# Performance work log

Measured on AMD Instinct MI355X. Metric: run time of the kernel, lower is better.

The kernel has to match this reference:

```python
import jax, jax.numpy as jnp
import numpy as np
import itertools

B, T, C, H = 2, 2048, 1024, 8
HD = C // H  # head_dim = 128


def _head_dirs():
    # 8 trigrams = vertices of cube {-1,+1}^3, L2-normalized (norm sqrt(3))
    signs = [-1.0, 1.0]
    tri = np.array(list(itertools.product(signs, repeat=3)), dtype=np.float32)
    tri = tri / np.linalg.norm(tri, axis=1, keepdims=True)
    return jnp.asarray(tri[:H])  # [H, 3]


def setup_inputs() -> dict:
    key = jax.random.key(0)
    ks = jax.random.split(key, 5)
    w = lambda k, sh: jax.random.normal(k, sh, dtype=jnp.float32) * 0.02
    return {
        "x": jax.random.normal(ks[0], (B, T, C), dtype=jnp.float32),
        "Wq": w(ks[1], (H * 3, C)),
        "Wk": w(ks[2], (H * 3, C)),
        "Wv": w(ks[3], (C, C)),
        "Wo": w(ks[4], (C, C)),
        "scale": jnp.asarray(1.0 / np.sqrt(3.0), dtype=jnp.float32),
    }


def reference(x, Wq, Wk, Wv, Wo, scale):
    Bb, Tt, Cc = x.shape
    dirs = _head_dirs()  # [H, 3] constant buffer
    # tiny 3-dim per-head Q/K projections
    q3 = (x @ Wq.T).reshape(Bb, Tt, H, 3).transpose(0, 2, 1, 3)  # [B,H,T,3]
    k3 = (x @ Wk.T).reshape(Bb, Tt, H, 3).transpose(0, 2, 1, 3)  # [B,H,T,3]
    v = (x @ Wv.T).reshape(Bb, Tt, H, HD).transpose(0, 2, 1, 3)  # [B,H,T,HD]
    # projections of q/k onto each head's trigram direction
    q_on_dir = jnp.einsum('bhtd,hd->bht', q3, dirs)  # [B,H,T]
    k_on_dir = jnp.einsum('bhtd,hd->bht', k3, dirs)  # [B,H,T]
    # scores = scaled 3-dim dot product + geometric outer-product bias
    scores = jnp.einsum('bhtd,bhsd->bhts', q3, k3) * scale \
        + q_on_dir[..., :, None] * k_on_dir[..., None, :]  # [B,H,T,T]
    causal = jnp.tril(jnp.ones((Tt, Tt), dtype=bool))
    scores = jnp.where(causal, scores, -jnp.inf)
    attn = jax.nn.softmax(scores, axis=-1)
    out = jnp.einsum('bhts,bhsd->bhtd', attn, v)  # [B,H,T,HD]
    out = out.transpose(0, 2, 1, 3).reshape(Bb, Tt, Cc)
    return out @ Wo.T
```

## Files before the change

kernel.cpp:

```cpp
#include <hip/hip_runtime.h>
#include <hip/hip_bf16.h>

#define B_  2
#define T_  2048
#define C_  1024
#define H_  8
#define HD_ 128
#define M_  (B_*T_)

typedef short  bf16x8 __attribute__((ext_vector_type(8)));
typedef float  f32x4  __attribute__((ext_vector_type(4)));
typedef unsigned short u16x8 __attribute__((ext_vector_type(8)));
typedef unsigned int   u32x4 __attribute__((ext_vector_type(4)));

typedef const __attribute__((address_space(1))) void* gas_ptr;
typedef __attribute__((address_space(3))) void*       las_ptr;

#define L2E_ 1.4426950408889634f

static __device__ __forceinline__ unsigned short f2bf(float f) {
    unsigned int u = __float_as_uint(f);
    u += 0x7fffu + ((u >> 16) & 1u);
    return (unsigned short)(u >> 16);
}
static __device__ __forceinline__ unsigned int rne_u32(float f) {
    unsigned int u = __float_as_uint(f);
    return u + 0x7fffu + ((u >> 16) & 1u);
}
static __device__ __forceinline__ float bf2f(unsigned short u) {
    return __uint_as_float(((unsigned int)u) << 16);
}
static __device__ __forceinline__ float exp2_fast(float x) {
#if __has_builtin(__builtin_amdgcn_exp2f)
    return __builtin_amdgcn_exp2f(x);
#else
    return exp2f(x);
#endif
}

__global__ __launch_bounds__(256) void k_proj_qk(const float* __restrict__ x,
                                                 const float* __restrict__ Wq,
                                                 const float* __restrict__ Wk,
                                                 const float* __restrict__ Wv,
                                                 const float* __restrict__ Wo,
                                                 const float* __restrict__ scale_p,
                                                 float* __restrict__ qt,
                                                 float* __restrict__ kt,
                                                 unsigned short* __restrict__ xbf,
                                                 unsigned short* __restrict__ wvbf,
                                                 unsigned short* __restrict__ wobf) {
    __shared__ __align__(16) float wl[48][260];
    __shared__ __align__(16) float xl[16][260];
    __shared__ float res[16][48];
    const int tid  = threadIdx.x;

    if (blockIdx.x >= (M_ / 16)) {
        int i = (blockIdx.x - M_ / 16) * 256 + tid;
        const float* src; unsigned short* dst; int off;
        if (i < 262144) { src = Wv; dst = wvbf; off = i; }
        else            { src = Wo; dst = wobf; off = i - 262144; }
        float4 v = reinterpret_cast<const float4*>(src)[off];
        ushort4 o;
        o.x = f2bf(v.x); o.y = f2bf(v.y); o.z = f2bf(v.z); o.w = f2bf(v.w);
        reinterpret_cast<ushort4*>(dst)[off] = o;
        return;
    }

    const int row0 = blockIdx.x << 4;
    const int r    = tid >> 4, sub = tid & 15;
    float a0 = 0.f, a1 = 0.f, a2 = 0.f;

    for (int ch = 0; ch < 4; ++ch) {
        const int k0 = ch * 256;
        #pragma unroll
        for (int i = 0; i < 12; ++i) {
            int fi = i * 256 + tid;
            int wr = fi >> 6, wc = (fi & 63) * 4;
            const float* src = (wr < 24) ? (Wq + (size_t)wr * C_) : (Wk + (size_t)(wr - 24) * C_);
            *reinterpret_cast<float4*>(&wl[wr][wc]) = *reinterpret_cast<const float4*>(src + k0 + wc);
        }
        #pragma unroll
        for (int i = 0; i < 4; ++i) {
            int fi = i * 256 + tid;
            int xr = fi >> 6, xc = (fi & 63) * 4;
            size_t goff = (size_t)(row0 + xr) * C_ + k0 + xc;
            float4 xv = *reinterpret_cast<const float4*>(x + goff);
            *reinterpret_cast<float4*>(&xl[xr][xc]) = xv;
            ushort4 o;
            o.x = f2bf(xv.x); o.y = f2bf(xv.y); o.z = f2bf(xv.z); o.w = f2bf(xv.w);
            *reinterpret_cast<ushort4*>(xbf + goff) = o;
        }
        __syncthreads();
        const int oc = sub * 3;
        #pragma unroll 4
        for (int k = 0; k < 256; k += 4) {
            float4 xv = *reinterpret_cast<const float4*>(&xl[r][k]);
            float4 w0 = *reinterpret_cast<const float4*>(&wl[oc + 0][k]);
            float4 w1 = *reinterpret_cast<const float4*>(&wl[oc + 1][k]);
            float4 w2 = *reinterpret_cast<const float4*>(&wl[oc + 2][k]);
            a0 += xv.x * w0.x + xv.y * w0.y + xv.z * w0.z + xv.w * w0.w;
            a1 += xv.x * w1.x + xv.y * w1.y + xv.z * w1.z + xv.w * w1.w;
            a2 += xv.x * w2.x + xv.y * w2.y + xv.z * w2.z + xv.w * w2.w;
        }
        __syncthreads();
    }
    res[r][sub * 3 + 0] = a0;
    res[r][sub * 3 + 1] = a1;
    res[r][sub * 3 + 2] = a2;
    __syncthreads();

    {
        const int rr = tid >> 4, s2 = tid & 15;
        const int isK = s2 >> 3, h = s2 & 7;
        const float r3 = 0.57735026918962576f;
        float d0 = (h & 4) ? r3 : -r3;
        float d1 = (h & 2) ? r3 : -r3;
        float d2 = (h & 1) ? r3 : -r3;
        const float* v3 = &res[rr][isK * 24 + h * 3];
        float a = v3[0], b = v3[1], c = v3[2];
        float ond = a * d0 + b * d1 + c * d2;
        float sc = scale_p[0];
        float4 ov = isK ? make_float4(a, b, c, ond)
                        : make_float4(a * sc * L2E_, b * sc * L2E_, c * sc * L2E_, ond * L2E_);
        float* dst = isK ? kt : qt;
        int grow = row0 + rr;
        int b_ = grow >> 11, t_idx = grow & (T_ - 1);
        reinterpret_cast<float4*>(dst)[(size_t)(b_ * H_ + h) * T_ + t_idx] = ov;
    }
}

template <int MODE>
__global__ __launch_bounds__(256) void k_gemm128x64(const unsigned short* __restrict__ A,
                                                    const unsigned short* __restrict__ Bw,
                                                    void* __restrict__ Cout,
                                                    int Mdim, int Ndim, int Kdim) {
    __shared__ __align__(16) unsigned short lds_a[8][128][8];
    __shared__ __align__(16) unsigned short lds_b[8][64][8];
    const int tid = threadIdx.x;
    const int nbn = Ndim >> 6;
    const int cpx = (int)gridDim.x >> 3;
    const int bidx = (blockIdx.x & 7) * cpx + (blockIdx.x >> 3);
    const int bm = (bidx / nbn) << 7;
    const int bn = (bidx % nbn) << 6;
    const int w = tid >> 6, l = tid & 63;
    const int wm = (w >> 1) << 6, wn = (w & 1) << 5;
    const int lh = l & 15, lq = l >> 4;

    f32x4 acc[4][2];
    #pragma unroll
    for (int i = 0; i < 4; ++i)
        #pragma unroll
        for (int j = 0; j < 2; ++j)
            acc[i][j] = (f32x4){0.f, 0.f, 0.f, 0.f};

    for (int k0 = 0; k0 < Kdim; k0 += 64) {
        #pragma unroll
        for (int p = 0; p < 4; ++p) {
            int flat = p * 256 + tid;
            int kq = flat >> 7, row = flat & 127;
            __builtin_amdgcn_global_load_lds((gas_ptr)(A + (size_t)(bm + row) * Kdim + k0 + kq * 8),
                (las_ptr)(&lds_a[0][0][0] + (size_t)flat * 8), 16, 0, 0);
        }
        #pragma unroll
        for (int p = 0; p < 2; ++p) {
            int flat = p * 256 + tid;
            int kq = flat >> 6, row = flat & 63;
            __builtin_amdgcn_global_load_lds((gas_ptr)(Bw + (size_t)(bn + row) * Kdim + k0 + kq * 8),
                (las_ptr)(&lds_b[0][0][0] + (size_t)flat * 8), 16, 0, 0);
        }
        __syncthreads();

        #pragma unroll
        for (int kk = 0; kk < 2; ++kk) {
            bf16x8 af[4], bfr[2];
            #pragma unroll
            for (int f = 0; f < 4; ++f)
                af[f] = *reinterpret_cast<const bf16x8*>(&lds_a[lq + 4 * kk][wm + f * 16 + lh][0]);
            #pragma unroll
            for (int f = 0; f < 2; ++f)
                bfr[f] = *reinterpret_cast<const bf16x8*>(&lds_b[lq + 4 * kk][wn + f * 16 + lh][0]);
            #pragma unroll
            for (int i = 0; i < 4; ++i)
                #pragma unroll
                for (int j = 0; j < 2; ++j)
                    acc[i][j] = __builtin_amdgcn_mfma_f32_16x16x32_bf16(af[i], bfr[j], acc[i][j], 0, 0, 0);
        }
        __syncthreads();
    }

    if constexpr (MODE == 0) {
        float* Cf = (float*)Cout;
        #pragma unroll
        for (int i = 0; i < 4; ++i) {
            int rbase = bm + wm + i * 16 + lq * 4;
            #pragma unroll
            for (int j = 0; j < 2; ++j) {
                int cidx = bn + wn + j * 16 + lh;
                #pragma unroll
                for (int r = 0; r < 4; ++r)
                    Cf[(size_t)(rbase + r) * Ndim + cidx] = acc[i][j][r];
            }
        }
    } else {
        __shared__ unsigned short ldsT[128][72];
        #pragma unroll
        for (int i = 0; i < 4; ++i)
            #pragma unroll
            for (int j = 0; j < 2; ++j)
                #pragma unroll
                for (int r = 0; r < 4; ++r)
                    ldsT[wm + i * 16 + lq * 4 + r][wn + j * 16 + lh] = f2bf(acc[i][j][r]);
        __syncthreads();
        unsigned short* vt_out = (unsigned short*)Cout;
        int c = tid & 63, part = tid >> 6;
        int b = bm >> 11, t0 = bm & (T_ - 1);
        unsigned short* dst = vt_out + ((size_t)b * C_ + bn + c) * T_ + t0 + part * 32;
        #pragma unroll
        for (int jj = 0; jj < 4; ++jj) {
            u16x8 v;
            #pragma unroll
            for (int k = 0; k < 8; ++k) v[k] = ldsT[part * 32 + jj * 8 + k][c];
            *reinterpret_cast<u16x8*>(dst + jj * 8) = v;
        }
    }
}

__global__ __launch_bounds__(256) void k_attn64(
        const float4* __restrict__ qt, const float4* __restrict__ kt,
        const unsigned short* __restrict__ vt,
        unsigned short* __restrict__ mpart,
        float2* __restrict__ mlbuf,
        int nsp, int lg2nsp) {
    __shared__ __align__(16) unsigned short lv[2][8192];
    __shared__ __align__(16) float4 lk[2][64];
    const int tid = threadIdx.x;
    const int w = tid >> 6, l = tid & 63;
    const int lh = l & 15, lg = l >> 4;
    const int bid = blockIdx.x;
    const int qb = 31 - (bid >> (4 + lg2nsp));
    const int sp = (bid >> 4) & (nsp - 1);
    const int bh = bid & 15;
    const int q0 = qb << 6;
    const int qrow = q0 + 4 * lh + w;
    const int nt = qb + 1;

    const float4* qtb = qt + (size_t)bh * T_;
    const float4* ktb = kt + (size_t)bh * T_;
    const unsigned short* vtb = vt + (size_t)bh * HD_ * T_;

    const unsigned short* vsrc[4];
    #pragma unroll
    for (int i = 0; i < 4; ++i) {
        int f = i * 256 + tid;
        vsrc[i] = vtb + (size_t)((((f >> 6) & 7) * 16) + (f & 15)) * T_
                      + ((f >> 9) << 5) + ((f >> 4) & 3) * 8;
    }

#define STAGE(ST, BUF) do {                                                    \
    int s0_ = (ST) << 6;                                                       \
    __builtin_amdgcn_global_load_lds((gas_ptr)(vsrc[0] + s0_),                 \
        (las_ptr)(&lv[BUF][0] + (size_t)(0 * 256 + tid) * 8), 16, 0, 0);       \
    __builtin_amdgcn_global_load_lds((gas_ptr)(vsrc[1] + s0_),                 \
        (las_ptr)(&lv[BUF][0] + (size_t)(1 * 256 + tid) * 8), 16, 0, 0);       \
    __builtin_amdgcn_global_load_lds((gas_ptr)(vsrc[2] + s0_),                 \
        (las_ptr)(&lv[BUF][0] + (size_t)(2 * 256 + tid) * 8), 16, 0, 0);       \
    __builtin_amdgcn_global_load_lds((gas_ptr)(vsrc[3] + s0_),                 \
        (las_ptr)(&lv[BUF][0] + (size_t)(3 * 256 + tid) * 8), 16, 0, 0);       \
    __builtin_amdgcn_global_load_lds((gas_ptr)(ktb + s0_ + l),                 \
        (las_ptr)(&lk[BUF][0]), 16, 0, 0);                                     \
} while (0)

    const float4 q4 = qtb[qrow];
    f32x4 acc[8];
    #pragma unroll
    for (int n = 0; n < 8; ++n) acc[n] = (f32x4){0.f, 0.f, 0.f, 0.f};
    float m = -1e30f, lsum = 0.f;

    if (sp < nt)       STAGE(sp, 0);
    if (sp + nsp < nt) STAGE(sp + nsp, 1);
    __syncthreads();

    int buf = 0;
    for (int st = sp; st < nt; st += nsp) {
        const int s0 = st << 6;
        const int c0 = s0 + lg * 8;
        const int c1 = s0 + 32 + lg * 8;

        float p[16];
        if (st != qb) {
            #pragma unroll
            for (int jj = 0; jj < 8; ++jj) {
                float4 k4 = lk[buf][lg * 8 + jj];
                p[jj] = fmaf(q4.x, k4.x, fmaf(q4.y, k4.y, fmaf(q4.z, k4.z, q4.w * k4.w)));
            }
            #pragma unroll
            for (int jj = 0; jj < 8; ++jj) {
                float4 k4 = lk[buf][32 + lg * 8 + jj];
                p[8 + jj] = fmaf(q4.x, k4.x, fmaf(q4.y, k4.y, fmaf(q4.z, k4.z, q4.w * k4.w)));
            }
        } else {
            #pragma unroll
            for (int jj = 0; jj < 8; ++jj) {
                float4 k4 = lk[buf][lg * 8 + jj];
                float sc = fmaf(q4.x, k4.x, fmaf(q4.y, k4.y, fmaf(q4.z, k4.z, q4.w * k4.w)));
                p[jj] = (c0 + jj > qrow) ? -1e30f : sc;
            }
            #pragma unroll
            for (int jj = 0; jj < 8; ++jj) {
                float4 k4 = lk[buf][32 + lg * 8 + jj];
                float sc = fmaf(q4.x, k4.x, fmaf(q4.y, k4.y, fmaf(q4.z, k4.z, q4.w * k4.w)));
                p[8 + jj] = (c1 + jj > qrow) ? -1e30f : sc;
            }
        }

        float ma = fmaxf(fmaxf(p[0], p[1]), p[2]);
        float mb = fmaxf(fmaxf(p[3], p[4]), p[5]);
        float mc = fmaxf(fmaxf(p[6], p[7]), p[8]);
        float md = fmaxf(fmaxf(p[9], p[10]), p[11]);
        float me = fmaxf(fmaxf(p[12], p[13]), p[14]);
        float mt = fmaxf(fmaxf(fmaxf(ma, mb), fmaxf(mc, md)), fmaxf(me, p[15]));
        mt = fmaxf(mt, __shfl_xor(mt, 16));
        mt = fmaxf(mt, __shfl_xor(mt, 32));
        if (__any(mt > m + 8.f)) {
            float mnew = fmaxf(m, mt);
            float corr = exp2_fast(m - mnew);
            m = mnew;
            lsum *= corr;
            float cc0 = __shfl(corr, 4 * lg + 0);
            float cc1 = __shfl(corr, 4 * lg + 1);
            float cc2 = __shfl(corr, 4 * lg + 2);
            float cc3 = __shfl(corr, 4 * lg + 3);
            #pragma unroll
            for (int n = 0; n < 8; ++n) {
                acc[n][0] *= cc0; acc[n][1] *= cc1; acc[n][2] *= cc2; acc[n][3] *= cc3;
            }
        }
        #pragma unroll
        for (int jj = 0; jj < 16; ++jj)
            p[jj] = exp2_fast(p[jj] - m);
        float sa = (p[0] + p[1] + p[2]) + (p[3] + p[4] + p[5]);
        float sb = (p[6] + p[7] + p[8]) + (p[9] + p[10] + p[11]);
        float ps = sa + sb + ((p[12] + p[13] + p[14]) + p[15]);
        ps += __shfl_xor(ps, 16);
        ps += __shfl_xor(ps, 32);
        lsum += ps;

        u32x4 w0, w1;
        #pragma unroll
        for (int i = 0; i < 4; ++i) {
            w0[i] = __builtin_amdgcn_perm(rne_u32(p[2 * i + 1]), rne_u32(p[2 * i]), 0x07060302u);
            w1[i] = __builtin_amdgcn_perm(rne_u32(p[8 + 2 * i + 1]), rne_u32(p[8 + 2 * i]), 0x07060302u);
        }
        bf16x8 pa0 = __builtin_bit_cast(bf16x8, w0);
        bf16x8 pa1 = __builtin_bit_cast(bf16x8, w1);

        #pragma unroll
        for (int n = 0; n < 8; ++n) {
            bf16x8 vf = *reinterpret_cast<const bf16x8*>(&lv[buf][(size_t)(n * 64 + lg * 16 + lh) * 8]);
            acc[n] = __builtin_amdgcn_mfma_f32_16x16x32_bf16(pa0, vf, acc[n], 0, 0, 0);
        }
        #pragma unroll
        for (int n = 0; n < 8; ++n) {
            bf16x8 vf = *reinterpret_cast<const bf16x8*>(&lv[buf][(size_t)(512 + n * 64 + lg * 16 + lh) * 8]);
            acc[n] = __builtin_amdgcn_mfma_f32_16x16x32_bf16(pa1, vf, acc[n], 0, 0, 0);
        }

        __syncthreads();
        if (st + 2 * nsp < nt) STAGE(st + 2 * nsp, buf);
        buf ^= 1;
    }
#undef STAGE

    unsigned short* mp = mpart + (size_t)(sp * 16 + bh) * T_ * HD_;
    #pragma unroll
    for (int n = 0; n < 8; ++n) {
        #pragma unroll
        for (int r = 0; r < 4; ++r) {
            int row = q0 + 16 * lg + 4 * r + w;
            mp[(size_t)row * HD_ + n * 16 + lh] = f2bf(acc[n][r]);
        }
    }
    if (lg == 0)
        mlbuf[(size_t)(sp * 16 + bh) * T_ + qrow] = make_float2(m, lsum);
}

__global__ __launch_bounds__(256) void k_combine(const unsigned short* __restrict__ mpart,
                                                 const float2* __restrict__ mlbuf,
                                                 unsigned short* __restrict__ attnbf,
                                                 int nsp) {
    int idx = blockIdx.x * 256 + threadIdx.x;
    int bh = idx >> 16;
    int rem = idx & 65535;
    int t = rem >> 5, d0 = (rem & 31) * 4;
    float mg = -1e30f, den = 0.f;
    float ax = 0.f, ay = 0.f, az = 0.f, aw = 0.f;
    for (int s = 0; s < nsp; ++s) {
        float2 ml = mlbuf[(size_t)(s * 16 + bh) * T_ + t];
        ushort4 a = *reinterpret_cast<const ushort4*>(
            mpart + ((size_t)(s * 16 + bh) * T_ + t) * HD_ + d0);
        float mn = fmaxf(mg, ml.x);
        float cOld = exp2_fast(mg - mn);
        float cNew = exp2_fast(ml.x - mn);
        den = den * cOld + ml.y * cNew;
        ax = ax * cOld + bf2f(a.x) * cNew;
        ay = ay * cOld + bf2f(a.y) * cNew;
        az = az * cOld + bf2f(a.z) * cNew;
        aw = aw * cOld + bf2f(a.w) * cNew;
        mg = mn;
    }
    float inv = 1.f / den;
    int b = bh >> 3, h = bh & 7;
    ushort4 o;
    o.x = f2bf(ax * inv); o.y = f2bf(ay * inv);
    o.z = f2bf(az * inv); o.w = f2bf(aw * inv);
    *reinterpret_cast<ushort4*>(attnbf + ((size_t)(b * T_ + t) * C_ + h * HD_ + d0)) = o;
}

extern "C" void kernel_launch(void* const* d_in, const int* in_sizes, int n_in,
                              void* d_out, int out_size, void* d_ws, size_t ws_size,
                              hipStream_t stream) {
    const float* x     = (const float*)d_in[0];
    const float* Wq    = (const float*)d_in[1];
    const float* Wk    = (const float*)d_in[2];
    const float* Wv    = (const float*)d_in[3];
    const float* Wo    = (const float*)d_in[4];
    const float* scale = (const float*)d_in[5];
    float* out = (float*)d_out;

    const int nsp    = (ws_size >= 46137344) ? 4 : 2;
    const int lg2nsp = (nsp == 4) ? 2 : 1;

    char* ws = (char*)d_ws;
    size_t o = (size_t)nsp * 8388608;
    unsigned short* mpart  = (unsigned short*)(ws);
    unsigned short* xbf    = (unsigned short*)(ws);
    unsigned short* wvbf   = (unsigned short*)(ws + 8388608);
    float*          qt     = (float*)(ws + o);
    float*          kt     = (float*)(ws + o + 524288);
    unsigned short* vt     = (unsigned short*)(ws + o + 1048576);
    unsigned short* attnbf = (unsigned short*)(ws + o + 1048576);
    unsigned short* wobf   = (unsigned short*)(ws + o + 9437184);
    float2*         mlbuf  = (float2*)(ws + o + 11534336);

    k_proj_qk<<<M_ / 16 + 2048, 256, 0, stream>>>(x, Wq, Wk, Wv, Wo, scale,
                                                  qt, kt, xbf, wvbf, wobf);

    k_gemm128x64<2><<<(M_ / 128) * (C_ / 64), 256, 0, stream>>>(xbf, wvbf, (void*)vt, M_, C_, C_);

    k_attn64<<<32 * nsp * 16, 256, 0, stream>>>(
        reinterpret_cast<const float4*>(qt), reinterpret_cast<const float4*>(kt), vt,
        mpart, mlbuf, nsp, lg2nsp);

    k_combine<<<4096, 256, 0, stream>>>(mpart, mlbuf, attnbf, nsp);

    k_gemm128x64<0><<<(M_ / 128) * (C_ / 64), 256, 0, stream>>>(attnbf, wobf, (void*)out, M_, C_, C_);
}
```

Baseline: 123.7 us.

## Shrink GEMM tiles to 64x64, early-exit empty attention splits, vectorize combine

The GEMM tile drops from 128x64 to 64x64, doubling the grid to 1024 blocks so the 256 CUs have more work to spread across, at the cost of less data reuse per block. Attention blocks whose split index has no key tiles now return immediately instead of running empty. The combine kernel reads only the splits that hold data for each row and handles 8 elements per thread with 16-byte loads and stores, halving the thread count. Together these target occupancy and wasted launch work across three kernels.

```diff
diff --git a/kernel.cpp b/kernel.cpp
--- a/kernel.cpp
+++ b/kernel.cpp
@@ -130,34 +130,34 @@
 }
 
 template <int MODE>
-__global__ __launch_bounds__(256) void k_gemm128x64(const unsigned short* __restrict__ A,
-                                                    const unsigned short* __restrict__ Bw,
-                                                    void* __restrict__ Cout,
-                                                    int Mdim, int Ndim, int Kdim) {
-    __shared__ __align__(16) unsigned short lds_a[8][128][8];
+__global__ __launch_bounds__(256) void k_gemm64(const unsigned short* __restrict__ A,
+                                                const unsigned short* __restrict__ Bw,
+                                                void* __restrict__ Cout,
+                                                int Mdim, int Ndim, int Kdim) {
+    __shared__ __align__(16) unsigned short lds_a[8][64][8];
     __shared__ __align__(16) unsigned short lds_b[8][64][8];
     const int tid = threadIdx.x;
     const int nbn = Ndim >> 6;
     const int cpx = (int)gridDim.x >> 3;
     const int bidx = (blockIdx.x & 7) * cpx + (blockIdx.x >> 3);
-    const int bm = (bidx / nbn) << 7;
+    const int bm = (bidx / nbn) << 6;
     const int bn = (bidx % nbn) << 6;
     const int w = tid >> 6, l = tid & 63;
-    const int wm = (w >> 1) << 6, wn = (w & 1) << 5;
+    const int wm = (w >> 1) << 5, wn = (w & 1) << 5;
     const int lh = l & 15, lq = l >> 4;
 
-    f32x4 acc[4][2];
-    #pragma unroll
-    for (int i = 0; i < 4; ++i)
+    f32x4 acc[2][2];
+    #pragma unroll
+    for (int i = 0; i < 2; ++i)
         #pragma unroll
         for (int j = 0; j < 2; ++j)
             acc[i][j] = (f32x4){0.f, 0.f, 0.f, 0.f};
 
     for (int k0 = 0; k0 < Kdim; k0 += 64) {
         #pragma unroll
-        for (int p = 0; p < 4; ++p) {
+        for (int p = 0; p < 2; ++p) {
             int flat = p * 256 + tid;
-            int kq = flat >> 7, row = flat & 127;
+            int kq = flat >> 6, row = flat & 63;
             __builtin_amdgcn_global_load_lds((gas_ptr)(A + (size_t)(bm + row) * Kdim + k0 + kq * 8),
                 (las_ptr)(&lds_a[0][0][0] + (size_t)flat * 8), 16, 0, 0);
         }
@@ -172,15 +172,15 @@
 
         #pragma unroll
         for (int kk = 0; kk < 2; ++kk) {
-            bf16x8 af[4], bfr[2];
-            #pragma unroll
-            for (int f = 0; f < 4; ++f)
+            bf16x8 af[2], bfr[2];
+            #pragma unroll
+            for (int f = 0; f < 2; ++f)
                 af[f] = *reinterpret_cast<const bf16x8*>(&lds_a[lq + 4 * kk][wm + f * 16 + lh][0]);
             #pragma unroll
             for (int f = 0; f < 2; ++f)
                 bfr[f] = *reinterpret_cast<const bf16x8*>(&lds_b[lq + 4 * kk][wn + f * 16 + lh][0]);
             #pragma unroll
-            for (int i = 0; i < 4; ++i)
+            for (int i = 0; i < 2; ++i)
                 #pragma unroll
                 for (int j = 0; j < 2; ++j)
                     acc[i][j] = __builtin_amdgcn_mfma_f32_16x16x32_bf16(af[i], bfr[j], acc[i][j], 0, 0, 0);
@@ -191,7 +191,7 @@
     if constexpr (MODE == 0) {
         float* Cf = (float*)Cout;
         #pragma unroll
-        for (int i = 0; i < 4; ++i) {
+        for (int i = 0; i < 2; ++i) {
             int rbase = bm + wm + i * 16 + lq * 4;
             #pragma unroll
             for (int j = 0; j < 2; ++j) {
@@ -202,9 +202,9 @@
             }
         }
     } else {
-        __shared__ unsigned short ldsT[128][72];
-        #pragma unroll
-        for (int i = 0; i < 4; ++i)
+        __shared__ unsigned short ldsT[64][72];
+        #pragma unroll
+        for (int i = 0; i < 2; ++i)
             #pragma unroll
             for (int j = 0; j < 2; ++j)
                 #pragma unroll
@@ -214,12 +214,12 @@
         unsigned short* vt_out = (unsigned short*)Cout;
         int c = tid & 63, part = tid >> 6;
         int b = bm >> 11, t0 = bm & (T_ - 1);
-        unsigned short* dst = vt_out + ((size_t)b * C_ + bn + c) * T_ + t0 + part * 32;
-        #pragma unroll
-        for (int jj = 0; jj < 4; ++jj) {
+        unsigned short* dst = vt_out + ((size_t)b * C_ + bn + c) * T_ + t0 + part * 16;
+        #pragma unroll
+        for (int jj = 0; jj < 2; ++jj) {
             u16x8 v;
             #pragma unroll
-            for (int k = 0; k < 8; ++k) v[k] = ldsT[part * 32 + jj * 8 + k][c];
+            for (int k = 0; k < 8; ++k) v[k] = ldsT[part * 16 + jj * 8 + k][c];
             *reinterpret_cast<u16x8*>(dst + jj * 8) = v;
         }
     }
@@ -244,6 +244,8 @@
     const int qrow = q0 + 4 * lh + w;
     const int nt = qb + 1;
 
+    if (sp >= nt) return;
+
     const float4* qtb = qt + (size_t)bh * T_;
     const float4* ktb = kt + (size_t)bh * T_;
     const unsigned short* vtb = vt + (size_t)bh * HD_ * T_;
@@ -276,7 +278,7 @@
     for (int n = 0; n < 8; ++n) acc[n] = (f32x4){0.f, 0.f, 0.f, 0.f};
     float m = -1e30f, lsum = 0.f;
 
-    if (sp < nt)       STAGE(sp, 0);
+    STAGE(sp, 0);
     if (sp + nsp < nt) STAGE(sp + nsp, 1);
     __syncthreads();
 
@@ -389,31 +391,33 @@
                                                  unsigned short* __restrict__ attnbf,
                                                  int nsp) {
     int idx = blockIdx.x * 256 + threadIdx.x;
-    int bh = idx >> 16;
-    int rem = idx & 65535;
-    int t = rem >> 5, d0 = (rem & 31) * 4;
+    int bh = idx >> 15;
+    int rem = idx & 32767;
+    int t = rem >> 4, d0 = (rem & 15) * 8;
+    int ns = (t >> 6) + 1; ns = (ns < nsp) ? ns : nsp;
     float mg = -1e30f, den = 0.f;
-    float ax = 0.f, ay = 0.f, az = 0.f, aw = 0.f;
-    for (int s = 0; s < nsp; ++s) {
+    float a[8];
+    #pragma unroll
+    for (int j = 0; j < 8; ++j) a[j] = 0.f;
+    for (int s = 0; s < ns; ++s) {
         float2 ml = mlbuf[(size_t)(s * 16 + bh) * T_ + t];
-        ushort4 a = *reinterpret_cast<const ushort4*>(
+        u16x8 v = *reinterpret_cast<const u16x8*>(
             mpart + ((size_t)(s * 16 + bh) * T_ + t) * HD_ + d0);
         float mn = fmaxf(mg, ml.x);
         float cOld = exp2_fast(mg - mn);
         float cNew = exp2_fast(ml.x - mn);
         den = den * cOld + ml.y * cNew;
-        ax = ax * cOld + bf2f(a.x) * cNew;
-        ay = ay * cOld + bf2f(a.y) * cNew;
-        az = az * cOld + bf2f(a.z) * cNew;
-        aw = aw * cOld + bf2f(a.w) * cNew;
+        #pragma unroll
+        for (int j = 0; j < 8; ++j)
+            a[j] = a[j] * cOld + bf2f((unsigned short)v[j]) * cNew;
         mg = mn;
     }
     float inv = 1.f / den;
     int b = bh >> 3, h = bh & 7;
-    ushort4 o;
-    o.x = f2bf(ax * inv); o.y = f2bf(ay * inv);
-    o.z = f2bf(az * inv); o.w = f2bf(aw * inv);
-    *reinterpret_cast<ushort4*>(attnbf + ((size_t)(b * T_ + t) * C_ + h * HD_ + d0)) = o;
+    u16x8 o;
+    #pragma unroll
+    for (int j = 0; j < 8; ++j) o[j] = f2bf(a[j] * inv);
+    *reinterpret_cast<u16x8*>(attnbf + ((size_t)(b * T_ + t) * C_ + h * HD_ + d0)) = o;
 }
 
 extern "C" void kernel_launch(void* const* d_in, const int* in_sizes, int n_in,
@@ -445,13 +449,13 @@
     k_proj_qk<<<M_ / 16 + 2048, 256, 0, stream>>>(x, Wq, Wk, Wv, Wo, scale,
                                                   qt, kt, xbf, wvbf, wobf);
 
-    k_gemm128x64<2><<<(M_ / 128) * (C_ / 64), 256, 0, stream>>>(xbf, wvbf, (void*)vt, M_, C_, C_);
+    k_gemm64<2><<<(M_ / 64) * (C_ / 64), 256, 0, stream>>>(xbf, wvbf, (void*)vt, M_, C_, C_);
 
     k_attn64<<<32 * nsp * 16, 256, 0, stream>>>(
         reinterpret_cast<const float4*>(qt), reinterpret_cast<const float4*>(kt), vt,
         mpart, mlbuf, nsp, lg2nsp);
 
-    k_combine<<<4096, 256, 0, stream>>>(mpart, mlbuf, attnbf, nsp);
-
-    k_gemm128x64<0><<<(M_ / 128) * (C_ / 64), 256, 0, stream>>>(attnbf, wobf, (void*)out, M_, C_, C_);
-}
+    k_combine<<<2048, 256, 0, stream>>>(mpart, mlbuf, attnbf, nsp);
+
+    k_gemm64<0><<<(M_ / 64) * (C_ / 64), 256, 0, stream>>>(attnbf, wobf, (void*)out, M_, C_, C_);
+}
```

Measured after the change: 138.6 us. 1.12x slower.
